# Kernel optimization log

Hardware: AMD Instinct MI355X
Metric: run time of the kernel (lower is better)

Reference implementation:

```python
import jax, jax.numpy as jnp
import numpy as np

B, T, NV, NH = 4, 128, 92, 4
N = NV + NH
D = 32          # d_species
H = 32          # free_nn_hidden
NUM_FORMS = 5
TOP_K = 8


def setup_inputs() -> dict:
    key = jax.random.key(0)
    ks = jax.random.split(key, 10)
    inp = {}
    inp["state"] = jax.random.uniform(ks[0], (B, T, N), dtype=jnp.float32)
    # learned parameters (per __init__)
    inp["species_emb"] = 0.1 * jax.random.normal(ks[1], (N, D), dtype=jnp.float32)
    inp["q_w"] = 0.05 * jax.random.normal(ks[2], (1 + D, D), dtype=jnp.float32)
    inp["q_b"] = jnp.zeros((D,), jnp.float32)
    inp["k_w"] = 0.05 * jax.random.normal(ks[3], (1 + D, D), dtype=jnp.float32)
    inp["k_b"] = jnp.zeros((D,), jnp.float32)
    inp["form_coefs"] = 0.05 * jax.random.normal(ks[4], (NUM_FORMS, N, N), dtype=jnp.float32)
    gates = -2.0 * jnp.ones((NUM_FORMS, N, N), jnp.float32)
    gates = gates.at[:, :NV, NV:].set(0.0)  # hidden->visible edges start open
    inp["form_gates_raw"] = gates
    inp["holling_alpha_raw"] = jnp.zeros((N,), jnp.float32)
    # free-form MLP: Linear(2+2D,H) -> GELU -> Linear(H,H) -> GELU -> Linear(H,1)
    inp["w1"] = 0.05 * jax.random.normal(ks[5], (2 + 2 * D, H), dtype=jnp.float32)
    inp["b1"] = jnp.zeros((H,), jnp.float32)
    inp["w2"] = 0.05 * jax.random.normal(ks[6], (H, H), dtype=jnp.float32)
    inp["b2"] = jnp.zeros((H,), jnp.float32)
    inp["w3"] = 0.05 * jax.random.normal(ks[7], (H, 1), dtype=jnp.float32)
    inp["b3"] = jnp.zeros((1,), jnp.float32)
    inp["r"] = jnp.zeros((N,), jnp.float32)
    return inp


def _forward(state, species_emb, q_w, q_b, k_w, k_b, form_coefs, form_gates_raw,
             holling_alpha_raw, w1, b1, w2, b2, w3, b3, r):
    Bc, Tc, Nc = state.shape
    d = species_emb.shape[1]
    gates = jax.nn.sigmoid(form_gates_raw)                  # (F,N,N)
    alpha = jax.nn.softplus(holling_alpha_raw) + 0.01       # (N,)

    xi = state[..., :, None]                                # (B,T,N,1) receiver i
    xj = state[..., None, :]                                # (B,T,1,N) sender j
    hol = xj / (1.0 + alpha * xj)                           # (B,T,1,N)
    f0 = jnp.broadcast_to(xj, (Bc, Tc, Nc, Nc))             # Linear
    f1 = xi * xj                                            # LV bilinear
    f2 = jnp.broadcast_to(hol, (Bc, Tc, Nc, Nc))            # Holling II linear
    f3 = xi * hol                                           # Holling II bilinear

    # Free NN over [x_i, x_j, s_i, s_j]: decompose first Linear to avoid the
    # (B,T,N,N,2+2D) concat; mathematically identical.
    w_xi, w_xj = w1[0], w1[1]                               # (H,), (H,)
    emb_i = species_emb @ w1[2:2 + d]                       # (N,H)
    emb_j = species_emb @ w1[2 + d:]                        # (N,H)
    h = (xi[..., None] * w_xi + xj[..., None] * w_xj
         + emb_i[None, None, :, None, :] + emb_j[None, None, None, :, :] + b1)
    h = jax.nn.gelu(h, approximate=False)
    h = jax.nn.gelu(h @ w2 + b2, approximate=False)
    f4 = (h @ w3 + b3)[..., 0]                              # (B,T,N,N)

    forms = jnp.stack([f0, f1, f2, f3, f4], axis=0)         # (F,B,T,N,N)
    w = (form_coefs * gates)[:, None, None]                 # (F,1,1,N,N)
    msgs = (w * forms).sum(axis=0)                          # (B,T,N,N)

    feats = jnp.concatenate(
        [state[..., None], jnp.broadcast_to(species_emb, (Bc, Tc, Nc, d))], axis=-1)
    q = feats @ q_w + q_b                                   # (B,T,N,D)
    k = feats @ k_w + k_b
    scores = jnp.einsum('btnd,btmd->btnm', q, k) / jnp.sqrt(jnp.float32(d))

    # top-k masked softmax over senders
    topv, _ = jax.lax.top_k(scores, TOP_K)
    thresh = topv[..., -1:]
    masked = jnp.where(scores >= thresh, scores, -jnp.inf)
    attn = jax.nn.softmax(masked, axis=-1)                  # (B,T,N,N)

    agg = (attn * msgs).sum(axis=-1)                        # (B,T,N)
    log_ratio = r + agg
    return log_ratio, attn


def reference(state, species_emb, q_w, q_b, k_w, k_b, form_coefs, form_gates_raw,
              holling_alpha_raw, w1, b1, w2, b2, w3, b3, r):
    return _forward(state, species_emb, q_w, q_b, k_w, k_b, form_coefs,
                    form_gates_raw, holling_alpha_raw, w1, b1, w2, b2, w3, b3, r)
```

## Files before the change

kernel.cpp:

```cpp
#include <hip/hip_runtime.h>
#include <math.h>

#define N_SP 96
#define D_EMB 32
#define H_MLP 32
#define NPAIR 9216
#define NBT 512
#define BROWS 16

#define WS_F_EMBI  0
#define WS_F_EMBJT 3072
#define WS_F_ALPHA 6176
#define WS_F_WG4   6272
#define WS_F_WG1   43136
#define WS_F_QG    52352
#define WS_F_KTG   1625216
#define WS_F_END   3214464

typedef __attribute__((ext_vector_type(8))) short bf16x8;
typedef __attribute__((ext_vector_type(4))) float f32x4;
typedef __attribute__((ext_vector_type(4))) unsigned u32x4;

__device__ __forceinline__ float gelu_fast(float x){
  float x2 = x * x;
  float z  = x * fmaf(x2, -0.1029438824f, -2.3022077325f);
  float e  = __builtin_amdgcn_exp2f(z);
  return x * __builtin_amdgcn_rcpf(1.0f + e);
}

__device__ __forceinline__ unsigned short f2bf(float f){
  unsigned u = __builtin_bit_cast(unsigned, f);
  unsigned r = (u + 0x7FFFu + ((u >> 16) & 1u)) >> 16;
  return (unsigned short)r;
}
__device__ __forceinline__ float bf2f(unsigned short s){
  unsigned u = ((unsigned)s) << 16;
  return __builtin_bit_cast(float, u);
}

__device__ __forceinline__ unsigned cvt_pk_bf16(float lo, float hi){
  unsigned r;
  asm("v_cvt_pk_bf16_f32 %0, %1, %2" : "=v"(r) : "v"(lo), "v"(hi));
  return r;
}

__global__ __launch_bounds__(256) void pre_all_kernel(
    const float* __restrict__ state,
    const float* __restrict__ emb,
    const float* __restrict__ qwg, const float* __restrict__ qbg,
    const float* __restrict__ kwg, const float* __restrict__ kbg,
    const float* __restrict__ w1, const float* __restrict__ b1,
    const float* __restrict__ har,
    const float* __restrict__ fc, const float* __restrict__ fg,
    float* __restrict__ wsf){
  const int blk = blockIdx.x;
  const int tid = threadIdx.x;

  if (blk < 2*NBT){
    const int bt   = blk >> 1;
    const int noff = (blk & 1) * 48;
    float* qg  = wsf + WS_F_QG  + bt*(N_SP*D_EMB);
    float* ktg = wsf + WS_F_KTG + bt*3104;
    for (int t = tid; t < 48*D_EMB; t += 256){
      const int n = noff + (t >> 5), d2 = t & 31;
      const float xn = state[bt*N_SP + n];
      const float* e = emb + n*D_EMB;
      float aq = __fmul_rn(xn, qwg[d2]);
      float ak = __fmul_rn(xn, kwg[d2]);
      #pragma unroll
      for (int u = 0; u < D_EMB; u++){
        aq = fmaf(e[u], qwg[(1+u)*D_EMB + d2], aq);
        ak = fmaf(e[u], kwg[(1+u)*D_EMB + d2], ak);
      }
      aq = __fadd_rn(aq, qbg[d2]);
      ak = __fadd_rn(ak, kbg[d2]);
      qg[n*D_EMB + d2] = aq;
      ktg[d2*97 + n]   = ak;
    }
  } else if (blk < 2*NBT + 24){
    const int gidx = (blk - 2*NBT)*256 + tid;
    const int n = gidx >> 6;
    const int t = gidx & 63;
    const int which = t >> 5, idx = t & 31;
    const float* e = emb + n * D_EMB;
    if (which == 0){
      float acc = b1[idx];
      #pragma unroll
      for (int u = 0; u < D_EMB; u++) acc = fmaf(e[u], w1[(2+u)*H_MLP + idx], acc);
      wsf[WS_F_EMBI + n*H_MLP + idx] = acc;
    } else {
      float acc = 0.f;
      #pragma unroll
      for (int u = 0; u < D_EMB; u++) acc = fmaf(e[u], w1[(2+D_EMB+u)*H_MLP + idx], acc);
      wsf[WS_F_EMBJT + idx*97 + n] = acc;
    }
    if (t == 0){
      float h = har[n];
      float sp = (h > 20.f) ? h : log1pf(expf(h));
      wsf[WS_F_ALPHA + n] = sp + 0.01f;
    }
  } else {
    int idx = (blk - 2*NBT - 24) * 256 + tid;
    if (idx < 5 * NPAIR){
      float g = 1.f / (1.f + expf(-fg[idx]));
      float v = fc[idx] * g;
      int f = idx / NPAIR;
      int p = idx - f * NPAIR;
      if (f < 4) wsf[WS_F_WG4 + 4*p + f] = v;
      else       wsf[WS_F_WG1 + p] = v;
    }
  }
}

__device__ __forceinline__ void np_score4(const float* __restrict__ qA,
                                          const float* __restrict__ qB,
                                          const float* kT, int j1, int j2,
                                          float* v0A, float* v0B,
                                          float* v1A, float* v1B){
  float A1[4], B1[4], A2[4], B2[4];
  #pragma unroll
  for (int l = 0; l < 4; l++){
    float k1v[8], k2v[8], qa[8], qb[8];
    #pragma unroll
    for (int m = 0; m < 8; m++){
      k1v[m] = kT[(4*m+l)*97 + j1];
      k2v[m] = kT[(4*m+l)*97 + j2];
      qa[m]  = qA[4*m+l];
      qb[m]  = qB[4*m+l];
    }
    float tA1 = __fadd_rn(__fmul_rn(qa[1],k1v[1]), __fmul_rn(qa[0],k1v[0]));
    float tB1 = __fadd_rn(__fmul_rn(qb[1],k1v[1]), __fmul_rn(qb[0],k1v[0]));
    float tA2 = __fadd_rn(__fmul_rn(qa[1],k2v[1]), __fmul_rn(qa[0],k2v[0]));
    float tB2 = __fadd_rn(__fmul_rn(qb[1],k2v[1]), __fmul_rn(qb[0],k2v[0]));
    #pragma unroll
    for (int m = 2; m < 8; m++){
      tA1 = __fadd_rn(__fmul_rn(qa[m],k1v[m]), tA1);
      tB1 = __fadd_rn(__fmul_rn(qb[m],k1v[m]), tB1);
      tA2 = __fadd_rn(__fmul_rn(qa[m],k2v[m]), tA2);
      tB2 = __fadd_rn(__fmul_rn(qb[m],k2v[m]), tB2);
    }
    A1[l]=tA1; B1[l]=tB1; A2[l]=tA2; B2[l]=tB2;
  }
  const float S = 5.65685424949238019521f;
  *v0A = __fdiv_rn(__fadd_rn(__fadd_rn(A1[0],A1[1]), __fadd_rn(A1[2],A1[3])), S);
  *v0B = __fdiv_rn(__fadd_rn(__fadd_rn(B1[0],B1[1]), __fadd_rn(B1[2],B1[3])), S);
  *v1A = __fdiv_rn(__fadd_rn(__fadd_rn(A2[0],A2[1]), __fadd_rn(A2[2],A2[3])), S);
  *v1B = __fdiv_rn(__fadd_rn(__fadd_rn(B2[0],B2[1]), __fadd_rn(B2[2],B2[3])), S);
}

__global__ __launch_bounds__(256) void main_kernel(
    const float* __restrict__ state, const float* __restrict__ rvec,
    const float* __restrict__ w2g, const float* __restrict__ b3g,
    const float* __restrict__ w1, const float* __restrict__ b2g,
    const float* __restrict__ w3g,
    const float* __restrict__ wsf,
    float* __restrict__ out_lr, float* __restrict__ out_attn){

  __shared__ float s_kT[3104];
  __shared__ unsigned short s_embjT16[3104];
  __shared__ __align__(16) float s_embi[BROWS*H_MLP];
  __shared__ float s_x[N_SP], s_hol[N_SP];
  __shared__ float s_wxi[H_MLP], s_wxj[H_MLP], s_b2[H_MLP], s_w3[H_MLP];
  __shared__ int   s_selj[4][2][16];
  __shared__ float s_msg[4][2][16];

  const int tid  = threadIdx.x;
  const int bt   = blockIdx.x / 6;
  const int roff = (blockIdx.x - 6*bt) * BROWS;
  const int wave = tid >> 6, lane = tid & 63;

  const float* ktg = wsf + WS_F_KTG + bt*3104;
  for (int t = tid; t < 3104; t += 256){
    s_kT[t]       = ktg[t];
    s_embjT16[t]  = f2bf(wsf[WS_F_EMBJT + t]);
  }
  for (int t = tid; t < BROWS*H_MLP; t += 256)
    s_embi[t] = wsf[WS_F_EMBI + roff*H_MLP + t];
  if (tid < N_SP){
    float x = state[bt*N_SP + tid];
    s_x[tid] = x;
    float al = wsf[WS_F_ALPHA + tid];
    s_hol[tid] = x / (1.f + al * x);
  }
  if (tid >= 96 && tid < 128){
    int u = tid - 96;
    s_wxi[u] = w1[u];
    s_wxj[u] = w1[H_MLP + u];
    s_b2[u]  = b2g[u];
    s_w3[u]  = w3g[u];
  }

  const float b3v = b3g[0];
  const float* wg4 = wsf + WS_F_WG4;
  const float* wg1 = wsf + WS_F_WG1;
  const float* qg  = wsf + WS_F_QG + bt*(N_SP*D_EMB);

  const int l15 = lane & 15;
  const int g16 = lane >> 4;
  const int kb  = g16 * 8;
  bf16x8 w2f0, w2f1;
  #pragma unroll
  for (int e = 0; e < 8; e++){
    w2f0[e] = (short)f2bf(w2g[(kb+e)*H_MLP + l15]);
    w2f1[e] = (short)f2bf(w2g[(kb+e)*H_MLP + 16 + l15]);
  }
  __syncthreads();

  const float LOG2E = 1.44269504088896340736f;
  const int j2 = (lane < 32) ? (64 + lane) : 95;

  for (int ir = 0; ir < 2; ir++){
    const int ilA = 4*wave + 2*ir, ilB = ilA + 1;
    const int iA  = roff + ilA,    iB  = roff + ilB;
    const int iAu = __builtin_amdgcn_readfirstlane(iA);
    const int iBu = __builtin_amdgcn_readfirstlane(iB);
    const float* qA = qg + iAu*D_EMB;
    const float* qB = qg + iBu*D_EMB;

    float v0A, v0B, v1A, v1B;
    np_score4(qA, qB, s_kT, lane, j2, &v0A, &v0B, &v1A, &v1B);

    unsigned k0A = __builtin_bit_cast(unsigned, v0A);
    k0A = (k0A >> 31) ? ~k0A : (k0A | 0x80000000u);
    unsigned k0B = __builtin_bit_cast(unsigned, v0B);
    k0B = (k0B >> 31) ? ~k0B : (k0B | 0x80000000u);
    unsigned k1A = 0u, k1B = 0u;
    if (lane < 32){
      unsigned uA = __builtin_bit_cast(unsigned, v1A);
      k1A = (uA >> 31) ? ~uA : (uA | 0x80000000u);
      unsigned uB = __builtin_bit_cast(unsigned, v1B);
      k1B = (uB >> 31) ? ~uB : (uB | 0x80000000u);
    }

    unsigned TA = 0u, TB = 0u;
    #pragma unroll
    for (int b = 31; b >= 0; --b){
      const unsigned bit = 1u << b;
      unsigned TcA = TA | bit;
      unsigned TcB = TB | bit;
      unsigned long long a0 = __ballot(k0A >= TcA);
      unsigned long long b0 = __ballot(k0B >= TcB);
      unsigned long long a1 = __ballot(k1A >= TcA);
      unsigned long long b1 = __ballot(k1B >= TcB);
      if (__popcll(a0) + __popcll(a1) >= 8) TA = TcA;
      if (__popcll(b0) + __popcll(b1) >= 8) TB = TcB;
    }

    unsigned long long mA0 = __ballot(k0A >= TA);
    unsigned long long mA1 = __ballot(k1A >= TA);
    unsigned long long mB0 = __ballot(k0B >= TB);
    unsigned long long mB1 = __ballot(k1B >= TB);
    const int cA0 = __popcll(mA0);
    const int cB0 = __popcll(mB0);
    int r0A = -1, r1A = -1, r0B = -1, r1B = -1;
    const unsigned long long ltm = (1ull << lane) - 1ull;
    if (k0A >= TA){
      r0A = __popcll(mA0 & ltm);
      if (r0A < 16) s_selj[wave][0][r0A] = lane;
    }
    if (lane < 32 && k1A >= TA){
      r1A = cA0 + __popcll(mA1 & ltm);
      if (r1A < 16) s_selj[wave][0][r1A] = 64 + lane;
    }
    if (k0B >= TB){
      r0B = __popcll(mB0 & ltm);
      if (r0B < 16) s_selj[wave][1][r0B] = lane;
    }
    if (lane < 32 && k1B >= TB){
      r1B = cB0 + __popcll(mB1 & ltm);
      if (r1B < 16) s_selj[wave][1][r1B] = 64 + lane;
    }
    asm volatile("s_waitcnt lgkmcnt(0)" ::: "memory");

    const int cntA = cA0 + __popcll(mA1);
    const int cntB = cB0 + __popcll(mB1);
    const int ncapA = (cntA < 16) ? cntA : 16;
    const int ncapB = (cntB < 16) ? cntB : 16;
    const int jPA = s_selj[wave][0][(l15 < ncapA) ? l15 : 0];
    const int jPB = s_selj[wave][1][(l15 < ncapB) ? l15 : 0];
    const float xjA = s_x[jPA], xjB = s_x[jPB];
    const float xiA = s_x[iA],  xiB = s_x[iB];

    float4 w4vA = {0,0,0,0}, w4vB = {0,0,0,0};
    float  w1vA = 0.f, w1vB = 0.f, hjpA = 0.f, hjpB = 0.f;
    if (lane < 16){
      const int pA = iA*N_SP + jPA;
      const int pB = iB*N_SP + jPB;
      w4vA = *(const float4*)&wg4[4*pA];
      w1vA = wg1[pA];
      hjpA = s_hol[jPA];
      w4vB = *(const float4*)&wg4[4*pB];
      w1vB = wg1[pB];
      hjpB = s_hol[jPB];
    }

    u32x4 hwA, hwB;
    #pragma unroll
    for (int e2 = 0; e2 < 4; e2++){
      const int u0 = kb + 2*e2, u1 = u0 + 1;
      const float wj0 = s_wxj[u0], wj1 = s_wxj[u1];
      const float bA0 = fmaf(xiA, s_wxi[u0], s_embi[ilA*H_MLP + u0]);
      const float bA1 = fmaf(xiA, s_wxi[u1], s_embi[ilA*H_MLP + u1]);
      const float bB0 = fmaf(xiB, s_wxi[u0], s_embi[ilB*H_MLP + u0]);
      const float bB1 = fmaf(xiB, s_wxi[u1], s_embi[ilB*H_MLP + u1]);
      float pA0 = gelu_fast(fmaf(xjA, wj0, bA0 + bf2f(s_embjT16[u0*97 + jPA])));
      float pA1 = gelu_fast(fmaf(xjA, wj1, bA1 + bf2f(s_embjT16[u1*97 + jPA])));
      float pB0 = gelu_fast(fmaf(xjB, wj0, bB0 + bf2f(s_embjT16[u0*97 + jPB])));
      float pB1 = gelu_fast(fmaf(xjB, wj1, bB1 + bf2f(s_embjT16[u1*97 + jPB])));
      hwA[e2] = cvt_pk_bf16(pA0, pA1);
      hwB[e2] = cvt_pk_bf16(pB0, pB1);
    }
    const bf16x8 hfA = __builtin_bit_cast(bf16x8, hwA);
    const bf16x8 hfB = __builtin_bit_cast(bf16x8, hwB);

    f32x4 a0A = {s_b2[4*g16+0], s_b2[4*g16+1], s_b2[4*g16+2], s_b2[4*g16+3]};
    f32x4 a1A = {s_b2[16+4*g16+0], s_b2[16+4*g16+1], s_b2[16+4*g16+2], s_b2[16+4*g16+3]};
    f32x4 a0B = a0A, a1B = a1A;
    a0A = __builtin_amdgcn_mfma_f32_16x16x32_bf16(w2f0, hfA, a0A, 0, 0, 0);
    a0B = __builtin_amdgcn_mfma_f32_16x16x32_bf16(w2f0, hfB, a0B, 0, 0, 0);
    a1A = __builtin_amdgcn_mfma_f32_16x16x32_bf16(w2f1, hfA, a1A, 0, 0, 0);
    a1B = __builtin_amdgcn_mfma_f32_16x16x32_bf16(w2f1, hfB, a1B, 0, 0, 0);

    float partA = 0.f, partB = 0.f;
    #pragma unroll
    for (int r = 0; r < 4; r++){
      const float w3v = s_w3[4*g16 + r];
      partA = fmaf(gelu_fast(a0A[r]), w3v, partA);
      partB = fmaf(gelu_fast(a0B[r]), w3v, partB);
    }
    #pragma unroll
    for (int r = 0; r < 4; r++){
      const float w3v = s_w3[16 + 4*g16 + r];
      partA = fmaf(gelu_fast(a1A[r]), w3v, partA);
      partB = fmaf(gelu_fast(a1B[r]), w3v, partB);
    }
    partA += __shfl_xor(partA, 16);
    partB += __shfl_xor(partB, 16);
    partA += __shfl_xor(partA, 32);
    partB += __shfl_xor(partB, 32);

    if (lane < 16){
      const float f4A = partA + b3v;
      const float f4B = partB + b3v;
      const float msgA = w4vA.x * xjA + w4vA.y * (xiA*xjA)
                       + w4vA.z * hjpA + w4vA.w * (xiA*hjpA) + w1vA * f4A;
      const float msgB = w4vB.x * xjB + w4vB.y * (xiB*xjB)
                       + w4vB.z * hjpB + w4vB.w * (xiB*hjpB) + w1vB * f4B;
      s_msg[wave][0][lane] = msgA;
      s_msg[wave][1][lane] = msgB;
    }
    asm volatile("s_waitcnt lgkmcnt(0)" ::: "memory");

    float e0A = (k0A >= TA) ? __builtin_amdgcn_exp2f(LOG2E*v0A) : 0.f;
    float e0B = (k0B >= TB) ? __builtin_amdgcn_exp2f(LOG2E*v0B) : 0.f;
    float e1A = 0.f, e1B = 0.f;
    if (lane < 32){
      if (k1A >= TA) e1A = __builtin_amdgcn_exp2f(LOG2E*v1A);
      if (k1B >= TB) e1B = __builtin_amdgcn_exp2f(LOG2E*v1B);
    }

    float m0A = (r0A >= 0 && r0A < 16) ? s_msg[wave][0][r0A] : 0.f;
    float m1A = (r1A >= 0 && r1A < 16) ? s_msg[wave][0][r1A] : 0.f;
    float m0B = (r0B >= 0 && r0B < 16) ? s_msg[wave][1][r0B] : 0.f;
    float m1B = (r1B >= 0 && r1B < 16) ? s_msg[wave][1][r1B] : 0.f;

    float numA = e0A * m0A;
    float numB = e0B * m0B;
    if (lane < 32){ numA += e1A * m1A; numB += e1B * m1B; }
    float denA = e0A + e1A;
    float denB = e0B + e1B;
    #pragma unroll
    for (int off = 32; off; off >>= 1){
      denA += __shfl_xor(denA, off);
      denB += __shfl_xor(denB, off);
      numA += __shfl_xor(numA, off);
      numB += __shfl_xor(numB, off);
    }
    float invA = 1.0f / denA;
    float invB = 1.0f / denB;
    float* arowA = out_attn + (size_t)(bt*N_SP + iA) * N_SP;
    float* arowB = out_attn + (size_t)(bt*N_SP + iB) * N_SP;
    arowA[lane] = e0A * invA;
    arowB[lane] = e0B * invB;
    if (lane < 32){
      arowA[64 + lane] = e1A * invA;
      arowB[64 + lane] = e1B * invB;
    }
    if (lane == 0){
      out_lr[bt*N_SP + iA] = rvec[iA] + numA * invA;
      out_lr[bt*N_SP + iB] = rvec[iB] + numB * invB;
    }
  }
}

extern "C" void kernel_launch(void* const* d_in, const int* in_sizes, int n_in,
                              void* d_out, int out_size, void* d_ws, size_t ws_size,
                              hipStream_t stream){
  const float* state = (const float*)d_in[0];
  const float* emb   = (const float*)d_in[1];
  const float* qw    = (const float*)d_in[2];
  const float* qb    = (const float*)d_in[3];
  const float* kw    = (const float*)d_in[4];
  const float* kb    = (const float*)d_in[5];
  const float* fc    = (const float*)d_in[6];
  const float* fg    = (const float*)d_in[7];
  const float* har   = (const float*)d_in[8];
  const float* w1    = (const float*)d_in[9];
  const float* b1    = (const float*)d_in[10];
  const float* w2    = (const float*)d_in[11];
  const float* b2    = (const float*)d_in[12];
  const float* w3    = (const float*)d_in[13];
  const float* b3    = (const float*)d_in[14];
  const float* rv    = (const float*)d_in[15];

  float* wsf = (float*)d_ws;
  float* out_lr   = (float*)d_out;
  float* out_attn = out_lr + NBT * N_SP;

  hipLaunchKernelGGL(pre_all_kernel, dim3(2*NBT + 24 + 180), dim3(256), 0, stream,
                     state, emb, qw, qb, kw, kb, w1, b1, har, fc, fg, wsf);
  hipLaunchKernelGGL(main_kernel, dim3(6*NBT), dim3(256), 0, stream,
                     state, rv, w2, b3, w1, b2, w3, wsf, out_lr, out_attn);
}
```

Baseline: 94.69 us.

## Fuse Q/K projection into main kernel, dropping global Q/K workspace round-trip

```diff
diff --git a/kernel.cpp b/kernel.cpp
--- a/kernel.cpp
+++ b/kernel.cpp
@@ -13,9 +13,6 @@
 #define WS_F_ALPHA 6176
 #define WS_F_WG4   6272
 #define WS_F_WG1   43136
-#define WS_F_QG    52352
-#define WS_F_KTG   1625216
-#define WS_F_END   3214464
 
 typedef __attribute__((ext_vector_type(8))) short bf16x8;
 typedef __attribute__((ext_vector_type(4))) float f32x4;
@@ -45,10 +42,7 @@
 }
 
 __global__ __launch_bounds__(256) void pre_all_kernel(
-    const float* __restrict__ state,
     const float* __restrict__ emb,
-    const float* __restrict__ qwg, const float* __restrict__ qbg,
-    const float* __restrict__ kwg, const float* __restrict__ kbg,
     const float* __restrict__ w1, const float* __restrict__ b1,
     const float* __restrict__ har,
     const float* __restrict__ fc, const float* __restrict__ fg,
@@ -56,29 +50,8 @@
   const int blk = blockIdx.x;
   const int tid = threadIdx.x;
 
-  if (blk < 2*NBT){
-    const int bt   = blk >> 1;
-    const int noff = (blk & 1) * 48;
-    float* qg  = wsf + WS_F_QG  + bt*(N_SP*D_EMB);
-    float* ktg = wsf + WS_F_KTG + bt*3104;
-    for (int t = tid; t < 48*D_EMB; t += 256){
-      const int n = noff + (t >> 5), d2 = t & 31;
-      const float xn = state[bt*N_SP + n];
-      const float* e = emb + n*D_EMB;
-      float aq = __fmul_rn(xn, qwg[d2]);
-      float ak = __fmul_rn(xn, kwg[d2]);
-      #pragma unroll
-      for (int u = 0; u < D_EMB; u++){
-        aq = fmaf(e[u], qwg[(1+u)*D_EMB + d2], aq);
-        ak = fmaf(e[u], kwg[(1+u)*D_EMB + d2], ak);
-      }
-      aq = __fadd_rn(aq, qbg[d2]);
-      ak = __fadd_rn(ak, kbg[d2]);
-      qg[n*D_EMB + d2] = aq;
-      ktg[d2*97 + n]   = ak;
-    }
-  } else if (blk < 2*NBT + 24){
-    const int gidx = (blk - 2*NBT)*256 + tid;
+  if (blk < 24){
+    const int gidx = blk*256 + tid;
     const int n = gidx >> 6;
     const int t = gidx & 63;
     const int which = t >> 5, idx = t & 31;
@@ -100,7 +73,7 @@
       wsf[WS_F_ALPHA + n] = sp + 0.01f;
     }
   } else {
-    int idx = (blk - 2*NBT - 24) * 256 + tid;
+    int idx = (blk - 24) * 256 + tid;
     if (idx < 5 * NPAIR){
       float g = 1.f / (1.f + expf(-fg[idx]));
       float v = fc[idx] * g;
@@ -150,6 +123,9 @@
 
 __global__ __launch_bounds__(256) void main_kernel(
     const float* __restrict__ state, const float* __restrict__ rvec,
+    const float* __restrict__ emb,
+    const float* __restrict__ qwg, const float* __restrict__ qbg,
+    const float* __restrict__ kwg, const float* __restrict__ kbg,
     const float* __restrict__ w2g, const float* __restrict__ b3g,
     const float* __restrict__ w1, const float* __restrict__ b2g,
     const float* __restrict__ w3g,
@@ -157,6 +133,7 @@
     float* __restrict__ out_lr, float* __restrict__ out_attn){
 
   __shared__ float s_kT[3104];
+  __shared__ __align__(16) float s_q[BROWS*D_EMB];
   __shared__ unsigned short s_embjT16[3104];
   __shared__ __align__(16) float s_embi[BROWS*H_MLP];
   __shared__ float s_x[N_SP], s_hol[N_SP];
@@ -169,11 +146,31 @@
   const int roff = (blockIdx.x - 6*bt) * BROWS;
   const int wave = tid >> 6, lane = tid & 63;
 
-  const float* ktg = wsf + WS_F_KTG + bt*3104;
-  for (int t = tid; t < 3104; t += 256){
-    s_kT[t]       = ktg[t];
-    s_embjT16[t]  = f2bf(wsf[WS_F_EMBJT + t]);
-  }
+  for (int t = tid; t < N_SP*D_EMB; t += 256){
+    const int n = t >> 5, d2 = t & 31;
+    const float xn = state[bt*N_SP + n];
+    const float* e = emb + n*D_EMB;
+    float ak = __fmul_rn(xn, kwg[d2]);
+    #pragma unroll
+    for (int u = 0; u < D_EMB; u++)
+      ak = fmaf(e[u], kwg[(1+u)*D_EMB + d2], ak);
+    ak = __fadd_rn(ak, kbg[d2]);
+    s_kT[d2*97 + n] = ak;
+  }
+  for (int t = tid; t < BROWS*D_EMB; t += 256){
+    const int nl = t >> 5, d2 = t & 31;
+    const int n  = roff + nl;
+    const float xn = state[bt*N_SP + n];
+    const float* e = emb + n*D_EMB;
+    float aq = __fmul_rn(xn, qwg[d2]);
+    #pragma unroll
+    for (int u = 0; u < D_EMB; u++)
+      aq = fmaf(e[u], qwg[(1+u)*D_EMB + d2], aq);
+    aq = __fadd_rn(aq, qbg[d2]);
+    s_q[nl*D_EMB + d2] = aq;
+  }
+  for (int t = tid; t < 3104; t += 256)
+    s_embjT16[t] = f2bf(wsf[WS_F_EMBJT + t]);
   for (int t = tid; t < BROWS*H_MLP; t += 256)
     s_embi[t] = wsf[WS_F_EMBI + roff*H_MLP + t];
   if (tid < N_SP){
@@ -193,7 +190,6 @@
   const float b3v = b3g[0];
   const float* wg4 = wsf + WS_F_WG4;
   const float* wg1 = wsf + WS_F_WG1;
-  const float* qg  = wsf + WS_F_QG + bt*(N_SP*D_EMB);
 
   const int l15 = lane & 15;
   const int g16 = lane >> 4;
@@ -212,10 +208,10 @@
   for (int ir = 0; ir < 2; ir++){
     const int ilA = 4*wave + 2*ir, ilB = ilA + 1;
     const int iA  = roff + ilA,    iB  = roff + ilB;
-    const int iAu = __builtin_amdgcn_readfirstlane(iA);
-    const int iBu = __builtin_amdgcn_readfirstlane(iB);
-    const float* qA = qg + iAu*D_EMB;
-    const float* qB = qg + iBu*D_EMB;
+    const int ilAu = __builtin_amdgcn_readfirstlane(ilA);
+    const int ilBu = __builtin_amdgcn_readfirstlane(ilB);
+    const float* qA = s_q + ilAu*D_EMB;
+    const float* qB = s_q + ilBu*D_EMB;
 
     float v0A, v0B, v1A, v1B;
     np_score4(qA, qB, s_kT, lane, j2, &v0A, &v0B, &v1A, &v1B);
@@ -417,8 +413,9 @@
   float* out_lr   = (float*)d_out;
   float* out_attn = out_lr + NBT * N_SP;
 
-  hipLaunchKernelGGL(pre_all_kernel, dim3(2*NBT + 24 + 180), dim3(256), 0, stream,
-                     state, emb, qw, qb, kw, kb, w1, b1, har, fc, fg, wsf);
+  hipLaunchKernelGGL(pre_all_kernel, dim3(24 + 180), dim3(256), 0, stream,
+                     emb, w1, b1, har, fc, fg, wsf);
   hipLaunchKernelGGL(main_kernel, dim3(6*NBT), dim3(256), 0, stream,
-                     state, rv, w2, b3, w1, b2, w3, wsf, out_lr, out_attn);
-}
+                     state, rv, emb, qw, qb, kw, kb, w2, b3, w1, b2, w3,
+                     wsf, out_lr, out_attn);
+}
```

Measured after the change: 113.1 us. 19.4% more time.
